# Kernel optimization log

Hardware: AMD Instinct MI355X
Metric: run time of the kernel (lower is better)

The kernel has to match this reference:

```python
import jax, jax.numpy as jnp
import numpy as np
from jax import lax

B, N, D = 8, 4096, 768
H, K, U, V = 12, 16, 4, 64   # heads, key_depth, intra_depth, lambda_query_size
L = 23                        # local_context_size (odd)
PAD = L // 2
EPS = 1e-5


def setup_inputs() -> dict:
    key = jax.random.key(0)
    ks = jax.random.split(key, 9)
    return {
        "x": jax.random.normal(ks[0], (B, N, D), dtype=jnp.float32),
        "Wq": jax.random.normal(ks[1], (H * K, D), dtype=jnp.float32) * 0.02,
        "Wk": jax.random.normal(ks[2], (K * U, D), dtype=jnp.float32) * 0.02,
        "Wv": jax.random.normal(ks[3], (V * U, D), dtype=jnp.float32) * 0.02,
        "gamma_q": 1.0 + 0.1 * jax.random.normal(ks[4], (H * K,), dtype=jnp.float32),
        "beta_q": 0.1 * jax.random.normal(ks[5], (H * K,), dtype=jnp.float32),
        "gamma_v": 1.0 + 0.1 * jax.random.normal(ks[6], (V * U,), dtype=jnp.float32),
        "beta_v": 0.1 * jax.random.normal(ks[7], (V * U,), dtype=jnp.float32),
        "rel_pos_embed": jax.random.normal(ks[8], (K, U, 1, L), dtype=jnp.float32),
    }


def _batchnorm1d(z, gamma, beta):
    # z: (b, c, n); training-mode BatchNorm1d (biased variance over batch+length)
    mean = jnp.mean(z, axis=(0, 2), keepdims=True)
    var = jnp.mean((z - mean) ** 2, axis=(0, 2), keepdims=True)
    zhat = (z - mean) * lax.rsqrt(var + EPS)
    return zhat * gamma[None, :, None] + beta[None, :, None]


def reference(x, Wq, Wk, Wv, gamma_q, beta_q, gamma_v, beta_v, rel_pos_embed):
    b, n, d = x.shape
    xT = jnp.swapaxes(x, 1, 2)                      # b d n
    q = jnp.einsum('od,bdn->bon', Wq, xT)           # b (h k) n
    k = jnp.einsum('od,bdn->bon', Wk, xT)           # b (k u) n
    v = jnp.einsum('od,bdn->bon', Wv, xT)           # b (v u) n
    q = _batchnorm1d(q, gamma_q, beta_q)
    v = _batchnorm1d(v, gamma_v, beta_v)
    q = q.reshape(b, H, K, n)                       # b h k n
    k = k.reshape(b, K, U, n).transpose(0, 2, 1, 3) # b u k n
    v = v.reshape(b, V, U, n).transpose(0, 2, 1, 3) # b u v n
    k = jax.nn.softmax(k, axis=-1)                  # softmax over positions
    lam_c = jnp.einsum('bukn,buvn->bkv', k, v)      # content lambda
    Yc = jnp.einsum('bhkn,bkv->bnhv', q, lam_c)
    # position lambda via local conv over positions: v (b,u,V,n) * W (K,u,1,L) -> (b,K,V,n)
    lam_p = lax.conv_general_dilated(
        v, rel_pos_embed, window_strides=(1, 1),
        padding=((0, 0), (PAD, PAD)),
        dimension_numbers=('NCHW', 'OIHW', 'NCHW'))
    Yp = jnp.einsum('bhkn,bkvn->bnhv', q, lam_p)
    Y = (Yc + Yp).reshape(b, n, H * V)
    return Y
```

## Files before the change

kernel.cpp:

```cpp
#include <hip/hip_runtime.h>
#include <hip/hip_bf16.h>

constexpr int B = 8, N = 4096, D = 768;
constexpr int H = 12, K = 16, U = 4, V = 64, L = 23, PAD = 11;
constexpr int CQ = 192;
constexpr int CK = 64;
constexpr int CV = 256;
constexpr int CT = 512;
constexpr int CV0 = CQ + CK;
constexpr float EPS = 1e-5f;

typedef _Float16 f16x8 __attribute__((ext_vector_type(8)));
typedef _Float16 f16x4 __attribute__((ext_vector_type(4)));
typedef _Float16 f16x2 __attribute__((ext_vector_type(2)));
typedef float    f32x4 __attribute__((ext_vector_type(4)));

#define GLOAD16(gp, lp) __builtin_amdgcn_global_load_lds( \
    (const __attribute__((address_space(1))) void*)(gp),  \
    (__attribute__((address_space(3))) void*)(lp), 16, 0, 0)

__device__ __forceinline__ f16x2 pkrtz(float a, float b) {
    return __builtin_bit_cast(f16x2, __builtin_amdgcn_cvt_pkrtz(a, b));
}

__device__ __forceinline__ f16x8 cvt8r(float4 a, float4 b) {
    f16x8 r;
    r[0] = (_Float16)a.x; r[1] = (_Float16)a.y; r[2] = (_Float16)a.z; r[3] = (_Float16)a.w;
    r[4] = (_Float16)b.x; r[5] = (_Float16)b.y; r[6] = (_Float16)b.z; r[7] = (_Float16)b.w;
    return r;
}

__global__ __launch_bounds__(256) void k_w16(
    const float* __restrict__ Wq, const float* __restrict__ Wk,
    const float* __restrict__ Wv, const float* __restrict__ rel,
    _Float16* __restrict__ Wh, _Float16* __restrict__ relSg)
{
    const int bid = blockIdx.x;
    const int tid = threadIdx.x;
    if (bid < 192) {
        const int idx = bid * 256 + tid;
        const int c = idx / 96, g = idx % 96;
        const float* src;
        if (c < CQ)       src = Wq + (size_t)c * D;
        else if (c < CV0) src = Wk + (size_t)(c - CQ) * D;
        else              src = Wv + (size_t)(c - CV0) * D;
        float4 a = *(const float4*)(src + g * 8);
        float4 b = *(const float4*)(src + g * 8 + 4);
        *(f16x8*)(Wh + (size_t)c * D + g * 8) = cvt8r(a, b);
    } else {
        const int base = ((bid - 192) * 256 + tid) * 8;
        f16x8 o;
        #pragma unroll
        for (int j = 0; j < 8; ++j) {
            const int e = base + j;
            const int jj = e & 31, kk = (e >> 5) & 15;
            const int uu = (e >> 9) & 3, dd = e >> 11;
            const int l = jj - dd;
            float v = (l >= 0 && l < L) ? rel[(kk * U + uu) * L + l] : 0.f;
            o[j] = (_Float16)v;
        }
        *(f16x8*)(relSg + base) = o;
    }
}

__global__ __launch_bounds__(512) void k_proj(
    const float* __restrict__ x, const _Float16* __restrict__ Wh,
    _Float16* __restrict__ Ph)
{
    __shared__ _Float16 As0[512 * 32], As1[512 * 32], As2[512 * 32];
    __shared__ float    Bs0[128 * 32], Bs1[128 * 32], Bs2[128 * 32];
    const int b  = blockIdx.z;
    const int bn = blockIdx.x * 128;
    const int tid  = threadIdx.x;
    const int lane = tid & 63;
    const int wave = tid >> 6;
    const int wr  = wave >> 1;
    const int wcn = wave & 1;
    const int fr = lane & 15, sl = lane >> 4;

    const int arow_l = lane >> 2;
    const int achk   = (lane & 3) ^ (arow_l & 3) ^ ((arow_l >> 2) & 3);
    const int brow_l = lane >> 3;
    const int bchk   = (lane & 7) ^ brow_l;

    const _Float16* Wbase = Wh;
    const float*    xbase = x + ((size_t)b * N + bn) * D;

    const int ca = sl ^ (fr & 3) ^ ((fr >> 2) & 3);
    const int mb = fr & 7;

    f32x4 acc[8][4] = {};

#define STAGE(Ap, Bp, kt) do {                                         \
        _Pragma("unroll")                                              \
        for (int j = 0; j < 4; ++j) {                                  \
            const int r0 = wave * 64 + j * 16;                         \
            GLOAD16(Wbase + (size_t)(r0 + arow_l) * D + (kt) + achk * 8, \
                    (Ap) + r0 * 32);                                   \
        }                                                              \
        _Pragma("unroll")                                              \
        for (int j = 0; j < 2; ++j) {                                  \
            const int r0 = wave * 16 + j * 8;                          \
            GLOAD16(xbase + (size_t)(r0 + brow_l) * D + (kt) + bchk * 4, \
                    (Bp) + r0 * 32);                                   \
        }                                                              \
    } while (0)

#define WAIT6  asm volatile("s_waitcnt vmcnt(6)" ::: "memory")
#define WAIT0  asm volatile("s_waitcnt vmcnt(0)" ::: "memory")
#define BAR    __builtin_amdgcn_s_barrier()
#define SCHED0 __builtin_amdgcn_sched_barrier(0)

#define PHASE(Ap, Bp, StageStmt, WaitStmt) do {                        \
        f16x8 af[8]; float4 pa[4], pb[4];                              \
        _Pragma("unroll")                                              \
        for (int mi = 0; mi < 8; ++mi) {                               \
            const int ra = wr * 128 + mi * 16 + fr;                    \
            af[mi] = *(const f16x8*)((Ap) + ra * 32 + ca * 8);         \
        }                                                              \
        _Pragma("unroll")                                              \
        for (int ni = 0; ni < 4; ++ni) {                               \
            const int rb = wcn * 64 + ni * 16 + fr;                    \
            pa[ni] = *(const float4*)((Bp) + rb * 32 + (((sl * 2) ^ mb) * 4)); \
            pb[ni] = *(const float4*)((Bp) + rb * 32 + (((sl * 2 + 1) ^ mb) * 4)); \
        }                                                              \
        StageStmt;                                                     \
        WaitStmt;                                                      \
        SCHED0; BAR;                                                   \
        f16x8 bfr[4];                                                  \
        _Pragma("unroll")                                              \
        for (int ni = 0; ni < 4; ++ni) {                               \
            f16x2 p0 = pkrtz(pa[ni].x, pa[ni].y);                      \
            f16x2 p1 = pkrtz(pa[ni].z, pa[ni].w);                      \
            f16x2 p2 = pkrtz(pb[ni].x, pb[ni].y);                      \
            f16x2 p3 = pkrtz(pb[ni].z, pb[ni].w);                      \
            f16x8 bv;                                                  \
            bv[0] = p0[0]; bv[1] = p0[1]; bv[2] = p1[0]; bv[3] = p1[1]; \
            bv[4] = p2[0]; bv[5] = p2[1]; bv[6] = p3[0]; bv[7] = p3[1]; \
            bfr[ni] = bv;                                              \
        }                                                              \
        __builtin_amdgcn_s_setprio(1);                                 \
        _Pragma("unroll")                                              \
        for (int mi = 0; mi < 8; ++mi)                                 \
            _Pragma("unroll")                                          \
            for (int ni = 0; ni < 4; ++ni)                             \
                acc[mi][ni] = __builtin_amdgcn_mfma_f32_16x16x32_f16(  \
                    af[mi], bfr[ni], acc[mi][ni], 0, 0, 0);            \
        __builtin_amdgcn_s_setprio(0);                                 \
        SCHED0; BAR;                                                   \
    } while (0)

    STAGE(As0, Bs0, 0);
    STAGE(As1, Bs1, 32);
    WAIT6;
    BAR;

    for (int t0 = 0; t0 < 21; t0 += 3) {
        const int kt = t0 * 32;
        PHASE(As0, Bs0, STAGE(As2, Bs2, kt + 64),  WAIT6);
        PHASE(As1, Bs1, STAGE(As0, Bs0, kt + 96),  WAIT6);
        PHASE(As2, Bs2, STAGE(As1, Bs1, kt + 128), WAIT6);
    }
    PHASE(As0, Bs0, STAGE(As2, Bs2, 736), WAIT6);
    PHASE(As1, Bs1, (void)0, WAIT0);
    PHASE(As2, Bs2, (void)0, (void)0);

#undef STAGE
#undef PHASE
#undef WAIT6
#undef WAIT0
#undef BAR
#undef SCHED0

    _Float16* Pb = Ph + (size_t)b * CT * N + bn;
    #pragma unroll
    for (int mi = 0; mi < 8; ++mi)
        #pragma unroll
        for (int ni = 0; ni < 4; ++ni)
            #pragma unroll
            for (int r = 0; r < 4; ++r) {
                const int row = wr * 128 + mi * 16 + sl * 4 + r;
                const int col = wcn * 64 + ni * 16 + fr;
                Pb[(size_t)row * N + col] = (_Float16)acc[mi][ni][r];
            }
}

__global__ __launch_bounds__(256) void k_stats(
    const _Float16* __restrict__ Ph,
    const float* __restrict__ gq, const float* __restrict__ bq,
    const float* __restrict__ gv, const float* __restrict__ bv,
    float* __restrict__ sArr, float* __restrict__ tArr,
    float* __restrict__ mxk, float* __restrict__ invk,
    float* __restrict__ lamC)
{
    const int bid = blockIdx.x;
    const int tid = threadIdx.x;

    if (bid < CQ + CV) {
        const int ci = bid;
        const int c  = (ci < CQ) ? ci : ci + CK;
        float g, be;
        if (ci < CQ) { g = gq[ci];      be = bq[ci]; }
        else         { g = gv[ci - CQ]; be = bv[ci - CQ]; }

        float s = 0.f, s2 = 0.f;
        for (int b = 0; b < B; ++b) {
            const _Float16* row = Ph + ((size_t)b * CT + c) * N;
            #pragma unroll
            for (int i = 0; i < 2; ++i) {
                f16x8 v = ((const f16x8*)row)[i * 256 + tid];
                #pragma unroll
                for (int j = 0; j < 8; ++j) {
                    float f = (float)v[j];
                    s += f; s2 += f * f;
                }
            }
        }
        #pragma unroll
        for (int off = 32; off; off >>= 1) {
            s  += __shfl_xor(s, off);
            s2 += __shfl_xor(s2, off);
        }
        __shared__ float ls[4], ls2[4];
        if ((tid & 63) == 0) { ls[tid >> 6] = s; ls2[tid >> 6] = s2; }
        __syncthreads();
        if (tid == 0) {
            float S = ls[0] + ls[1] + ls[2] + ls[3];
            float S2 = ls2[0] + ls2[1] + ls2[2] + ls2[3];
            const float invM = 1.0f / (float)(B * N);
            float mean = S * invM;
            float var  = S2 * invM - mean * mean;
            float sc   = g / sqrtf(var + EPS);
            sArr[c] = sc;
            tArr[c] = be - mean * sc;
        }
    } else {
        const int idx = bid - (CQ + CV);
        if (idx < 8) {
            ((float4*)lamC)[idx * 256 + tid] = float4{0.f, 0.f, 0.f, 0.f};
        }
        const int b = idx >> 6, kc = idx & 63;
        const _Float16* row = Ph + ((size_t)b * CT + CQ + kc) * N;
        float v[16];
        float m = -3.4e38f;
        #pragma unroll
        for (int i = 0; i < 2; ++i) {
            f16x8 t = ((const f16x8*)row)[i * 256 + tid];
            #pragma unroll
            for (int j = 0; j < 8; ++j) {
                v[i*8+j] = (float)t[j];
                m = fmaxf(m, v[i*8+j]);
            }
        }
        #pragma unroll
        for (int off = 32; off; off >>= 1) m = fmaxf(m, __shfl_xor(m, off));
        __shared__ float rA[4], rB[4];
        if ((tid & 63) == 0) rA[tid >> 6] = m;
        __syncthreads();
        m = fmaxf(fmaxf(rA[0], rA[1]), fmaxf(rA[2], rA[3]));
        float s = 0.f;
        #pragma unroll
        for (int i = 0; i < 16; ++i) s += __expf(v[i] - m);
        #pragma unroll
        for (int off = 32; off; off >>= 1) s += __shfl_xor(s, off);
        if ((tid & 63) == 0) rB[tid >> 6] = s;
        __syncthreads();
        if (tid == 0) {
            s = rB[0] + rB[1] + rB[2] + rB[3];
            mxk[b * CK + kc]  = m;
            invk[b * CK + kc] = 1.f / s;
        }
    }
}

__global__ __launch_bounds__(256) void k_mid(
    const _Float16* __restrict__ Ph, const float* __restrict__ mxk,
    const float* __restrict__ invk, const float* __restrict__ sArr,
    const float* __restrict__ tArr, float* __restrict__ lamC)
{
    __shared__ float Kt[128][20];
    __shared__ float Vt[128][67];
    const int bid = blockIdx.x;
    const int tid = threadIdx.x;
    const int cx = bid & 15, u = (bid >> 4) & 3, b = bid >> 6;
    const int chunk0 = cx * 256;
    const int vv = tid & 63, kg = tid >> 6;
    float acc[4] = {0.f, 0.f, 0.f, 0.f};

    const int kk = tid >> 4, sK = tid & 15;
    const float mm = mxk[b * CK + kk * U + u];
    const float iv = invk[b * CK + kk * U + u];

    for (int sc = 0; sc < 2; ++sc) {
        const int nbase = chunk0 + sc * 128;
        __syncthreads();
        {
            f16x8 v = *(const f16x8*)(Ph + ((size_t)b * CT + CQ + kk * U + u) * N
                                      + nbase + sK * 8);
            #pragma unroll
            for (int i = 0; i < 8; ++i)
                Kt[sK * 8 + i][kk] = __expf((float)v[i] - mm) * iv;
        }
        {
            #pragma unroll
            for (int it = 0; it < 4; ++it) {
                const int task = it * 256 + tid;
                const int vvv = task >> 4, sV = task & 15;
                const int c = CV0 + vvv * U + u;
                f16x8 v = *(const f16x8*)(Ph + ((size_t)b * CT + c) * N
                                          + nbase + sV * 8);
                const float sc2 = sArr[c], tt = tArr[c];
                #pragma unroll
                for (int i = 0; i < 8; ++i)
                    Vt[sV * 8 + i][vvv] = (float)v[i] * sc2 + tt;
            }
        }
        __syncthreads();
        #pragma unroll 4
        for (int n = 0; n < 128; ++n) {
            float4 kv = *(const float4*)&Kt[n][kg * 4];
            float vx = Vt[n][vv];
            acc[0] += kv.x * vx; acc[1] += kv.y * vx;
            acc[2] += kv.z * vx; acc[3] += kv.w * vx;
        }
    }
    #pragma unroll
    for (int j = 0; j < 4; ++j)
        atomicAdd(&lamC[((size_t)b * K + kg * 4 + j) * V + vv], acc[j]);
}

__global__ __launch_bounds__(512) void k_out(
    const _Float16* __restrict__ Ph, const _Float16* __restrict__ relSg,
    const float* __restrict__ lamC, const float* __restrict__ sArr,
    const float* __restrict__ tArr, float* __restrict__ Y)
{
    constexpr int NT = 32;
    constexpr int VST = 72;
    constexpr int QST = 196;
    __shared__ _Float16 vsegT[256 * VST];
    __shared__ _Float16 qtile[NT * QST];

    const int b  = blockIdx.y;
    const int n0 = blockIdx.x * NT;
    const int tid  = threadIdx.x;
    const int lane = tid & 63;
    const int wave = tid >> 6;
    const int fr = lane & 15;
    const int sl = lane >> 4;

    #pragma unroll
    for (int it = 0; it < 4; ++it) {
        const int task = it * 512 + tid;
        const int ch = task >> 3, s = task & 7;
        const int c = CV0 + ch;
        const int row = (ch & 3) * 64 + (ch >> 2);
        const int nbase = n0 - 16 + s * 8;
        const float sc = sArr[c], tt = tArr[c];
        const bool full = (nbase >= 0) && (nbase + 8 <= N);
        f16x8 v{};
        if (full)
            v = *(const f16x8*)(Ph + ((size_t)b * CT + c) * N + nbase);
        #pragma unroll
        for (int i = 0; i < 8; ++i) {
            const int np = s * 8 - 5 + i;
            if (np < 0 || np >= 56) continue;
            float val = 0.f;
            if (full) {
                val = (float)v[i] * sc + tt;
            } else {
                const int n = nbase + i;
                if (n >= 0 && n < N)
                    val = (float)Ph[((size_t)b * CT + c) * N + n] * sc + tt;
            }
            vsegT[row * VST + np] = (_Float16)val;
        }
    }
    for (int task = tid; task < CQ * 4; task += 512) {
        const int ch = task >> 2, s = task & 3;
        f16x8 v = *(const f16x8*)(Ph + ((size_t)b * CT + ch) * N + n0 + s * 8);
        const float sc = sArr[ch], tt = tArr[ch];
        #pragma unroll
        for (int i = 0; i < 8; ++i)
            qtile[(s * 8 + i) * QST + ch] = (_Float16)((float)v[i] * sc + tt);
    }
    const int vg = wave & 3;
    const int nb = (wave >> 2) * 16;
    float lc[4];
    #pragma unroll
    for (int r = 0; r < 4; ++r)
        lc[r] = lamC[(size_t)b * K * V + (sl * 4 + r) * V + vg * 16 + fr];
    __syncthreads();

    for (int dlt = 0; dlt < 8; ++dlt) {
        f16x8 aU[4];
        #pragma unroll
        for (int u = 0; u < 4; ++u)
            aU[u] = *(const f16x8*)(relSg + ((dlt * 4 + u) * 16 + fr) * 32 + sl * 8);
        #pragma unroll
        for (int rep = 0; rep < 2; ++rep) {
            const int A  = nb + rep * 8;
            const int nn = A + dlt;
            f32x4 acc = {lc[0], lc[1], lc[2], lc[3]};
            #pragma unroll
            for (int u = 0; u < 4; ++u) {
                f16x8 bf = *(const f16x8*)(vsegT + (u * 64 + vg * 16 + fr) * VST + A + sl * 8);
                acc = __builtin_amdgcn_mfma_f32_16x16x32_f16(aU[u], bf, acc, 0, 0, 0);
            }
            f16x4 lam16;
            #pragma unroll
            for (int r = 0; r < 4; ++r) lam16[r] = (_Float16)acc[r];
            f16x4 q4 = *(const f16x4*)(qtile + nn * QST + fr * 16 + sl * 4);
            f32x4 y = {0.f, 0.f, 0.f, 0.f};
            y = __builtin_amdgcn_mfma_f32_16x16x16f16(q4, lam16, y, 0, 0, 0);
            if (sl < 3) {
                float* yr = Y + ((size_t)b * N + n0 + nn) * (H * V) + vg * 16 + fr;
                #pragma unroll
                for (int r = 0; r < 4; ++r)
                    yr[(sl * 4 + r) * 64] = y[r];
            }
        }
    }
}

extern "C" void kernel_launch(void* const* d_in, const int* in_sizes, int n_in,
                              void* d_out, int out_size, void* d_ws, size_t ws_size,
                              hipStream_t stream)
{
    const float* x   = (const float*)d_in[0];
    const float* Wq  = (const float*)d_in[1];
    const float* Wk  = (const float*)d_in[2];
    const float* Wv  = (const float*)d_in[3];
    const float* gq  = (const float*)d_in[4];
    const float* bq  = (const float*)d_in[5];
    const float* gv  = (const float*)d_in[6];
    const float* bv  = (const float*)d_in[7];
    const float* rel = (const float*)d_in[8];
    float* Y = (float*)d_out;

    _Float16* Ph  = (_Float16*)d_ws;
    float* sArr = (float*)(Ph + (size_t)B * CT * N);
    float* tArr = sArr + CT;
    float* lamC = tArr + CT;
    float* mxk  = lamC + (size_t)B * K * V;
    float* invk = mxk + B * CK;
    _Float16* Wh = (_Float16*)(invk + B * CK);
    _Float16* relSg = Wh + (size_t)CT * D;

    k_w16  <<<dim3(192 + 8), 256, 0, stream>>>(Wq, Wk, Wv, rel, Wh, relSg);
    k_proj <<<dim3(N / 128, 1, B), 512, 0, stream>>>(x, Wh, Ph);
    k_stats<<<dim3(CQ + CV + B * CK), 256, 0, stream>>>(Ph, gq, bq, gv, bv,
                                                        sArr, tArr, mxk, invk, lamC);
    k_mid  <<<dim3(512), 256, 0, stream>>>(Ph, mxk, invk, sArr, tArr, lamC);
    k_out  <<<dim3(N / 32, B), 512, 0, stream>>>(Ph, relSg, lamC, sArr, tArr, Y);
}
```

Measured before the change: 107.1 us.

## Convert x to fp16 in registers and double-buffer projection GEMM LDS

The projection GEMM no longer copies fp32 x tiles straight into LDS. Each thread now loads its slice of x into registers, converts it to fp16, and writes it to an fp16 B buffer. The pipeline also drops from three LDS stages to two, with a simpler ping-pong loop. This halves the B-tile LDS footprint and removes the per-phase pack conversion in the MFMA loop. In exchange, the x loads go through registers and there is less prefetch depth to hide global latency.

```diff
diff --git a/kernel.cpp b/kernel.cpp
--- a/kernel.cpp
+++ b/kernel.cpp
@@ -67,8 +67,8 @@
     const float* __restrict__ x, const _Float16* __restrict__ Wh,
     _Float16* __restrict__ Ph)
 {
-    __shared__ _Float16 As0[512 * 32], As1[512 * 32], As2[512 * 32];
-    __shared__ float    Bs0[128 * 32], Bs1[128 * 32], Bs2[128 * 32];
+    __shared__ _Float16 As0[512 * 32], As1[512 * 32];
+    __shared__ _Float16 Bs0[128 * 32], Bs1[128 * 32];
     const int b  = blockIdx.z;
     const int bn = blockIdx.x * 128;
     const int tid  = threadIdx.x;
@@ -80,64 +80,53 @@
 
     const int arow_l = lane >> 2;
     const int achk   = (lane & 3) ^ (arow_l & 3) ^ ((arow_l >> 2) & 3);
-    const int brow_l = lane >> 3;
-    const int bchk   = (lane & 7) ^ brow_l;
+    const int tb   = tid >> 2;
+    const int tseg = tid & 3;
+    const int bchk = tseg ^ (tb & 3) ^ ((tb >> 2) & 3);
+    const float* xrow = x + ((size_t)b * N + bn + tb) * D + tseg * 8;
 
     const _Float16* Wbase = Wh;
-    const float*    xbase = x + ((size_t)b * N + bn) * D;
-
     const int ca = sl ^ (fr & 3) ^ ((fr >> 2) & 3);
-    const int mb = fr & 7;
 
     f32x4 acc[8][4] = {};
 
-#define STAGE(Ap, Bp, kt) do {                                         \
+#define STAGE_A(Ap, kt) do {                                           \
         _Pragma("unroll")                                              \
         for (int j = 0; j < 4; ++j) {                                  \
             const int r0 = wave * 64 + j * 16;                         \
             GLOAD16(Wbase + (size_t)(r0 + arow_l) * D + (kt) + achk * 8, \
                     (Ap) + r0 * 32);                                   \
         }                                                              \
-        _Pragma("unroll")                                              \
-        for (int j = 0; j < 2; ++j) {                                  \
-            const int r0 = wave * 16 + j * 8;                          \
-            GLOAD16(xbase + (size_t)(r0 + brow_l) * D + (kt) + bchk * 4, \
-                    (Bp) + r0 * 32);                                   \
-        }                                                              \
     } while (0)
 
-#define WAIT6  asm volatile("s_waitcnt vmcnt(6)" ::: "memory")
+#define WAIT4  asm volatile("s_waitcnt vmcnt(4)" ::: "memory")
 #define WAIT0  asm volatile("s_waitcnt vmcnt(0)" ::: "memory")
+#define LGKM0  asm volatile("s_waitcnt lgkmcnt(0)" ::: "memory")
 #define BAR    __builtin_amdgcn_s_barrier()
 #define SCHED0 __builtin_amdgcn_sched_barrier(0)
 
-#define PHASE(Ap, Bp, StageStmt, WaitStmt) do {                        \
-        f16x8 af[8]; float4 pa[4], pb[4];                              \
+#define PHASE2(Acur, Bcur, Anxt, Bnxt, ktn, STAGEON) do {              \
+        float4 xr0{}, xr1{};                                           \
+        if (STAGEON) {                                                 \
+            xr0 = *(const float4*)(xrow + (ktn));                      \
+            xr1 = *(const float4*)(xrow + (ktn) + 4);                  \
+            STAGE_A(Anxt, ktn);                                        \
+            WAIT4;         \
+            *(f16x8*)((Bnxt) + tb * 32 + bchk * 8) = cvt8r(xr0, xr1);  \
+        } else {                                                       \
+            WAIT0;                                                     \
+        }                                                              \
+        SCHED0; BAR;                                                   \
+        f16x8 af[8], bf[4];                                            \
+        _Pragma("unroll")                                              \
+        for (int ni = 0; ni < 4; ++ni) {                               \
+            const int rb = wcn * 64 + ni * 16 + fr;                    \
+            bf[ni] = *(const f16x8*)((Bcur) + rb * 32 + ca * 8);       \
+        }                                                              \
         _Pragma("unroll")                                              \
         for (int mi = 0; mi < 8; ++mi) {                               \
             const int ra = wr * 128 + mi * 16 + fr;                    \
-            af[mi] = *(const f16x8*)((Ap) + ra * 32 + ca * 8);         \
-        }                                                              \
-        _Pragma("unroll")                                              \
-        for (int ni = 0; ni < 4; ++ni) {                               \
-            const int rb = wcn * 64 + ni * 16 + fr;                    \
-            pa[ni] = *(const float4*)((Bp) + rb * 32 + (((sl * 2) ^ mb) * 4)); \
-            pb[ni] = *(const float4*)((Bp) + rb * 32 + (((sl * 2 + 1) ^ mb) * 4)); \
-        }                                                              \
-        StageStmt;                                                     \
-        WaitStmt;                                                      \
-        SCHED0; BAR;                                                   \
-        f16x8 bfr[4];                                                  \
-        _Pragma("unroll")                                              \
-        for (int ni = 0; ni < 4; ++ni) {                               \
-            f16x2 p0 = pkrtz(pa[ni].x, pa[ni].y);                      \
-            f16x2 p1 = pkrtz(pa[ni].z, pa[ni].w);                      \
-            f16x2 p2 = pkrtz(pb[ni].x, pb[ni].y);                      \
-            f16x2 p3 = pkrtz(pb[ni].z, pb[ni].w);                      \
-            f16x8 bv;                                                  \
-            bv[0] = p0[0]; bv[1] = p0[1]; bv[2] = p1[0]; bv[3] = p1[1]; \
-            bv[4] = p2[0]; bv[5] = p2[1]; bv[6] = p3[0]; bv[7] = p3[1]; \
-            bfr[ni] = bv;                                              \
+            af[mi] = *(const f16x8*)((Acur) + ra * 32 + ca * 8);       \
         }                                                              \
         __builtin_amdgcn_s_setprio(1);                                 \
         _Pragma("unroll")                                              \
@@ -145,30 +134,33 @@
             _Pragma("unroll")                                          \
             for (int ni = 0; ni < 4; ++ni)                             \
                 acc[mi][ni] = __builtin_amdgcn_mfma_f32_16x16x32_f16(  \
-                    af[mi], bfr[ni], acc[mi][ni], 0, 0, 0);            \
+                    af[mi], bf[ni], acc[mi][ni], 0, 0, 0);             \
         __builtin_amdgcn_s_setprio(0);                                 \
-        SCHED0; BAR;                                                   \
+        LGKM0; SCHED0; BAR;                                            \
     } while (0)
 
-    STAGE(As0, Bs0, 0);
-    STAGE(As1, Bs1, 32);
-    WAIT6;
-    BAR;
-
-    for (int t0 = 0; t0 < 21; t0 += 3) {
-        const int kt = t0 * 32;
-        PHASE(As0, Bs0, STAGE(As2, Bs2, kt + 64),  WAIT6);
-        PHASE(As1, Bs1, STAGE(As0, Bs0, kt + 96),  WAIT6);
-        PHASE(As2, Bs2, STAGE(As1, Bs1, kt + 128), WAIT6);
-    }
-    PHASE(As0, Bs0, STAGE(As2, Bs2, 736), WAIT6);
-    PHASE(As1, Bs1, (void)0, WAIT0);
-    PHASE(As2, Bs2, (void)0, (void)0);
-
-#undef STAGE
-#undef PHASE
-#undef WAIT6
+    {
+        float4 p0 = *(const float4*)(xrow);
+        float4 p1 = *(const float4*)(xrow + 4);
+        STAGE_A(As0, 0);
+        WAIT4;
+        *(f16x8*)(Bs0 + tb * 32 + bchk * 8) = cvt8r(p0, p1);
+        LGKM0;
+    }
+
+    for (int kt = 0; kt < D; kt += 64) {
+        PHASE2(As0, Bs0, As1, Bs1, kt + 32, true);
+        if (kt + 64 < D) {
+            PHASE2(As1, Bs1, As0, Bs0, kt + 64, true);
+        } else {
+            PHASE2(As1, Bs1, As0, Bs0, 0, false);
+        }
+    }
+#undef STAGE_A
+#undef PHASE2
+#undef WAIT4
 #undef WAIT0
+#undef LGKM0
 #undef BAR
 #undef SCHED0
 
```

New measurement: 187.4 us. 1.75x slower.
